# Optimization experiments

Measured on AMD Instinct MI355X. Metric: run time of the kernel, lower is better.

## Reference

```python
import jax, jax.numpy as jnp
import numpy as np

B, V, F, P = 16, 100000, 200000, 65536


def _sample_one(verts, faces, e1, e2, u):
    # verts: [V,3], faces: [F,3], e1/e2/u: [P]
    tris = verts[faces]                      # [F,3,3] irregular gather
    vec1 = tris[:, 1, :] - tris[:, 0, :]
    vec2 = tris[:, 2, :] - tris[:, 0, :]
    normals = jnp.cross(vec1, vec2)          # [F,3]
    areas = jnp.linalg.norm(normals, axis=1) / 2.0  # [F]
    # area-weighted categorical sampling via inverse CDF (deterministic given u)
    cdf = jnp.cumsum(areas)
    cdf = cdf / cdf[-1]
    idx = jnp.clip(jnp.searchsorted(jax.lax.stop_gradient(cdf), u), 0, F - 1)  # [P]
    sampled_tris = tris[idx]                 # [P,3,3]
    unit_normals = normals / (areas[:, None] * 2.0)
    sampled_normals = unit_normals[idx]      # [P,3]
    # barycentric weights (Osada et al.)
    s = jnp.sqrt(e1)
    w = jnp.stack([1.0 - s, (1.0 - e2) * s, e2 * s], axis=1)[:, :, None]  # [P,3,1]
    points = jnp.sum(sampled_tris * w, axis=1)  # [P,3]
    return points, sampled_normals


def setup_inputs() -> dict:
    key = jax.random.key(0)
    k1, k2, k3, k4, k5 = jax.random.split(key, 5)
    vertices_batch = jax.random.normal(k1, (B, V, 3), dtype=jnp.float32)
    faces_batch = jax.random.randint(k2, (B, F, 3), 0, V, dtype=jnp.int64)
    eps1 = jax.random.uniform(k3, (B, P), dtype=jnp.float32)
    eps2 = jax.random.uniform(k4, (B, P), dtype=jnp.float32)
    u = jax.random.uniform(k5, (B, P), dtype=jnp.float32)
    return {"vertices_batch": vertices_batch, "faces_batch": faces_batch,
            "eps1": eps1, "eps2": eps2, "u": u}


def reference(vertices_batch, faces_batch, eps1, eps2, u):
    points, normals = jax.vmap(_sample_one)(vertices_batch, faces_batch, eps1, eps2, u)
    return points, normals  # ([B,P,3], [B,P,3])
```

## Files before the change

kernel.cpp:

```cpp
#include <hip/hip_runtime.h>

#pragma clang fp contract(off)

#define NB 16
#define NV 100000
#define NF 200000
#define NP 65536

#define B16 16
#define NW0 12500
#define NW1 782
#define NW2 49
#define NW3 4

__device__ __forceinline__ void xcd_map(int p, int& batch, int& chunk) {
    int r = p & 15;
    batch = 2 * (r & 7) + (r >> 3);
    chunk = p >> 4;
}

__global__ void detect_kernel(const int* __restrict__ faces, int* __restrict__ flag) {
    __shared__ int any;
    if (threadIdx.x == 0) any = 0;
    __syncthreads();
    int acc = 0;
    for (int i = threadIdx.x; i < 4096; i += blockDim.x)
        acc |= faces[2 * i + 1];
    if (acc) atomicOr(&any, 1);
    __syncthreads();
    if (threadIdx.x == 0) flag[0] = (any == 0) ? 1 : 0;
}

__device__ __forceinline__ void load_face(const int* __restrict__ faces,
                                          long long fidx, int is64,
                                          int& i0, int& i1, int& i2) {
    if (is64) {
        const int* p = faces + fidx * 6;
        i0 = p[0]; i1 = p[2]; i2 = p[4];
    } else {
        const int* p = faces + fidx * 3;
        i0 = p[0]; i1 = p[1]; i2 = p[2];
    }
}

__global__ void area_kernel(const float* __restrict__ verts,
                            const int* __restrict__ faces,
                            const int* __restrict__ flag,
                            float* __restrict__ area) {
    int batch, chunk;
    xcd_map(blockIdx.x, batch, chunk);
    int i = chunk * 256 + threadIdx.x;
    if (i >= NF) return;
    int is64 = flag[0];
    size_t gid = (size_t)batch * NF + i;
    const float* vb = verts + (size_t)batch * NV * 3;
    int i0, i1, i2;
    load_face(faces, (long long)gid, is64, i0, i1, i2);
    float ax = vb[3 * i0 + 0], ay = vb[3 * i0 + 1], az = vb[3 * i0 + 2];
    float bx = vb[3 * i1 + 0], by = vb[3 * i1 + 1], bz = vb[3 * i1 + 2];
    float cx = vb[3 * i2 + 0], cy = vb[3 * i2 + 1], cz = vb[3 * i2 + 2];
    float v1x = bx - ax, v1y = by - ay, v1z = bz - az;
    float v2x = cx - ax, v2y = cy - ay, v2z = cz - az;
    float nx = fmaf(v1y, v2z, -(v1z * v2y));
    float ny = fmaf(v1z, v2x, -(v1x * v2z));
    float nz = fmaf(v1x, v2y, -(v1y * v2x));
    float ss = fmaf(nz, nz, fmaf(nx, nx, ny * ny));
    float nrm = sqrtf(ss);
    area[gid] = nrm / 2.0f;
}

__global__ void winscan_kernel(float* __restrict__ cdf, float* __restrict__ s0) {
    int batch, chunk;
    xcd_map(blockIdx.x, batch, chunk);
    int j = chunk * 256 + threadIdx.x;
    if (j >= NW0) return;
    float* base = cdf + (size_t)batch * NF + (size_t)j * B16;
    float run = 0.0f;
    #pragma unroll
    for (int p = 0; p < B16; ++p) { run = run + base[p]; base[p] = run; }
    s0[(size_t)batch * NW0 + j] = run;
}

__global__ void midscan16_kernel(const float* __restrict__ s0g, float* __restrict__ S0g) {
    __shared__ float t0[NW0];
    __shared__ float t1[NW1];
    __shared__ float t2[NW2];
    __shared__ float t3[NW3];
    int b = blockIdx.x;
    for (int i = threadIdx.x; i < NW0; i += blockDim.x)
        t0[i] = s0g[(size_t)b * NW0 + i];
    __syncthreads();
    for (int w = threadIdx.x; w < NW1; w += blockDim.x) {
        int st = w * B16, en = st + B16 < NW0 ? st + B16 : NW0;
        float run = 0.0f;
        for (int p = st; p < en; ++p) { run = run + t0[p]; t0[p] = run; }
        t1[w] = run;
    }
    __syncthreads();
    for (int w = threadIdx.x; w < NW2; w += blockDim.x) {
        int st = w * B16, en = st + B16 < NW1 ? st + B16 : NW1;
        float run = 0.0f;
        for (int p = st; p < en; ++p) { run = run + t1[p]; t1[p] = run; }
        t2[w] = run;
    }
    __syncthreads();
    for (int w = threadIdx.x; w < NW3; w += blockDim.x) {
        int st = w * B16, en = st + B16 < NW2 ? st + B16 : NW2;
        float run = 0.0f;
        for (int p = st; p < en; ++p) { run = run + t2[p]; t2[p] = run; }
        t3[w] = run;
    }
    __syncthreads();
    if (threadIdx.x == 0) {
        float run = 0.0f;
        for (int k = 0; k < NW3; ++k) { run = run + t3[k]; t3[k] = run; }
    }
    __syncthreads();
    for (int i = threadIdx.x; i < NW2; i += blockDim.x) {
        int w = i >> 4;
        float off = (w > 0) ? t3[w - 1] : 0.0f;
        t2[i] = off + t2[i];
    }
    __syncthreads();
    for (int i = threadIdx.x; i < NW1; i += blockDim.x) {
        int w = i >> 4;
        float off = (w > 0) ? t2[w - 1] : 0.0f;
        t1[i] = off + t1[i];
    }
    __syncthreads();
    for (int i = threadIdx.x; i < NW0; i += blockDim.x) {
        int w = i >> 4;
        float off = (w > 0) ? t1[w - 1] : 0.0f;
        t0[i] = off + t0[i];
    }
    __syncthreads();
    for (int i = threadIdx.x; i < NW0; i += blockDim.x)
        S0g[(size_t)b * NW0 + i] = t0[i];
}

__global__ void fused_norm_kernel(float* __restrict__ cdf,
                                  const float* __restrict__ s0,
                                  const float* __restrict__ S0) {
    int batch, chunk;
    xcd_map(blockIdx.x, batch, chunk);
    int i = chunk * 256 + threadIdx.x;
    if (i >= NF) return;
    const float* S0b = S0 + (size_t)batch * NW0;
    float total = S0b[NW0 - 2] + s0[(size_t)batch * NW0 + NW0 - 1];
    float rcp = 1.0f / total;
    int j = i >> 4;
    float off = (j > 0) ? S0b[j - 1] : 0.0f;
    float* p = cdf + (size_t)batch * NF + i;
    *p = (off + *p) * rcp;
}

__global__ void sample_kernel(const float* __restrict__ verts,
                              const int* __restrict__ faces,
                              const int* __restrict__ flag,
                              const float* __restrict__ e1,
                              const float* __restrict__ e2,
                              const float* __restrict__ u,
                              const float* __restrict__ cdf,
                              float* __restrict__ out) {
    int batch, chunk;
    xcd_map(blockIdx.x, batch, chunk);
    int li = chunk * 256 + threadIdx.x;
    int b = batch;
    int gid = (b << 16) + li;
    int is64 = flag[0];
    const float* c = cdf + (size_t)b * NF;

    float uv = u[gid];
    int low = 0, high = NF;
    #pragma unroll
    for (int it = 0; it < 18; ++it) {
        int mid = (low + high) >> 1;
        bool go_left = (uv <= c[mid]);
        low  = go_left ? low : mid;
        high = go_left ? mid : high;
    }
    int idx = high < NF - 1 ? high : NF - 1;

    const float* vb = verts + (size_t)b * NV * 3;
    int i0, i1, i2;
    load_face(faces, (long long)b * NF + idx, is64, i0, i1, i2);
    double ax = vb[3 * i0 + 0], ay = vb[3 * i0 + 1], az = vb[3 * i0 + 2];
    double bx = vb[3 * i1 + 0], by = vb[3 * i1 + 1], bz = vb[3 * i1 + 2];
    double cx = vb[3 * i2 + 0], cy = vb[3 * i2 + 1], cz = vb[3 * i2 + 2];

    double v1x = bx - ax, v1y = by - ay, v1z = bz - az;
    double v2x = cx - ax, v2y = cy - ay, v2z = cz - az;
    double nx = v1y * v2z - v1z * v2y;
    double ny = v1z * v2x - v1x * v2z;
    double nz = v1x * v2y - v1y * v2x;
    double ss = (nx * nx + ny * ny) + nz * nz;
    double nrm = sqrt(ss);
    double unx = nx / nrm, uny = ny / nrm, unz = nz / nrm;

    double s = sqrt((double)e1[gid]);
    double t = (double)e2[gid];
    double w0 = 1.0 - s;
    double w1 = (1.0 - t) * s;
    double w2 = t * s;
    double px = (ax * w0 + bx * w1) + cx * w2;
    double py = (ay * w0 + by * w1) + cy * w2;
    double pz = (az * w0 + bz * w1) + cz * w2;

    size_t po = (size_t)gid * 3;
    out[po + 0] = (float)px;
    out[po + 1] = (float)py;
    out[po + 2] = (float)pz;
    size_t no = (size_t)NB * NP * 3 + po;
    out[no + 0] = (float)unx;
    out[no + 1] = (float)uny;
    out[no + 2] = (float)unz;
}

extern "C" void kernel_launch(void* const* d_in, const int* in_sizes, int n_in,
                              void* d_out, int out_size, void* d_ws, size_t ws_size,
                              hipStream_t stream) {
    const float* verts = (const float*)d_in[0];
    const int*   faces = (const int*)d_in[1];
    const float* e1    = (const float*)d_in[2];
    const float* e2    = (const float*)d_in[3];
    const float* u     = (const float*)d_in[4];
    float* out = (float*)d_out;

    char* ws = (char*)d_ws;
    int*   flag = (int*)ws;
    float* cdf  = (float*)(ws + 512);
    float* s0   = (float*)(ws + 512 + (size_t)NB * NF * 4);
    float* S0   = (float*)(ws + 512 + (size_t)NB * NF * 4 + (size_t)NB * NW0 * 4);

    detect_kernel<<<1, 256, 0, stream>>>(faces, flag);

    area_kernel<<<16 * 782, 256, 0, stream>>>(verts, faces, flag, cdf);

    winscan_kernel<<<16 * 49, 256, 0, stream>>>(cdf, s0);

    midscan16_kernel<<<NB, 256, 0, stream>>>(s0, S0);

    fused_norm_kernel<<<16 * 782, 256, 0, stream>>>(cdf, s0, S0);

    sample_kernel<<<16 * 256, 256, 0, stream>>>(verts, faces, flag, e1, e2, u, cdf, out);
}
```

Baseline: 174.1 us.

## Fuse area and window scan; cache top binary-search levels in shared memory

Merges the area computation with the 16-element window prefix scan through shared memory, which removes one kernel launch and a read-modify-write pass over the area array. The sample kernel now builds, per block, a shared-memory table holding the first 12 levels of the implicit binary-search tree over the CDF. The first 12 search steps read that table instead of global memory, and only the last 6 steps touch global memory. The cost is that every block rebuilds the 4095-entry table with scattered global reads, and each block is only 256 threads, so this overhead is large relative to the searches it saves.

```diff
diff --git a/kernel.cpp b/kernel.cpp
--- a/kernel.cpp
+++ b/kernel.cpp
@@ -12,6 +12,9 @@
 #define NW1 782
 #define NW2 49
 #define NW3 4
+
+#define TREE_LVL 12
+#define TREE_N   (1 << TREE_LVL)
 
 __device__ __forceinline__ void xcd_map(int p, int& batch, int& chunk) {
     int r = p & 15;
@@ -43,42 +46,46 @@
     }
 }
 
-__global__ void area_kernel(const float* __restrict__ verts,
-                            const int* __restrict__ faces,
-                            const int* __restrict__ flag,
-                            float* __restrict__ area) {
+__global__ void area_prefix_kernel(const float* __restrict__ verts,
+                                   const int* __restrict__ faces,
+                                   const int* __restrict__ flag,
+                                   float* __restrict__ cdf,
+                                   float* __restrict__ s0) {
+    __shared__ float S[256];
     int batch, chunk;
     xcd_map(blockIdx.x, batch, chunk);
-    int i = chunk * 256 + threadIdx.x;
-    if (i >= NF) return;
-    int is64 = flag[0];
-    size_t gid = (size_t)batch * NF + i;
-    const float* vb = verts + (size_t)batch * NV * 3;
-    int i0, i1, i2;
-    load_face(faces, (long long)gid, is64, i0, i1, i2);
-    float ax = vb[3 * i0 + 0], ay = vb[3 * i0 + 1], az = vb[3 * i0 + 2];
-    float bx = vb[3 * i1 + 0], by = vb[3 * i1 + 1], bz = vb[3 * i1 + 2];
-    float cx = vb[3 * i2 + 0], cy = vb[3 * i2 + 1], cz = vb[3 * i2 + 2];
-    float v1x = bx - ax, v1y = by - ay, v1z = bz - az;
-    float v2x = cx - ax, v2y = cy - ay, v2z = cz - az;
-    float nx = fmaf(v1y, v2z, -(v1z * v2y));
-    float ny = fmaf(v1z, v2x, -(v1x * v2z));
-    float nz = fmaf(v1x, v2y, -(v1y * v2x));
-    float ss = fmaf(nz, nz, fmaf(nx, nx, ny * ny));
-    float nrm = sqrtf(ss);
-    area[gid] = nrm / 2.0f;
-}
-
-__global__ void winscan_kernel(float* __restrict__ cdf, float* __restrict__ s0) {
-    int batch, chunk;
-    xcd_map(blockIdx.x, batch, chunk);
-    int j = chunk * 256 + threadIdx.x;
-    if (j >= NW0) return;
-    float* base = cdf + (size_t)batch * NF + (size_t)j * B16;
-    float run = 0.0f;
-    #pragma unroll
-    for (int p = 0; p < B16; ++p) { run = run + base[p]; base[p] = run; }
-    s0[(size_t)batch * NW0 + j] = run;
+    int tid = threadIdx.x;
+    int i = chunk * 256 + tid;
+    bool valid = (i < NF);
+    float a = 0.0f;
+    if (valid) {
+        int is64 = flag[0];
+        size_t gid = (size_t)batch * NF + i;
+        const float* vb = verts + (size_t)batch * NV * 3;
+        int i0, i1, i2;
+        load_face(faces, (long long)gid, is64, i0, i1, i2);
+        float ax = vb[3 * i0 + 0], ay = vb[3 * i0 + 1], az = vb[3 * i0 + 2];
+        float bx = vb[3 * i1 + 0], by = vb[3 * i1 + 1], bz = vb[3 * i1 + 2];
+        float cx = vb[3 * i2 + 0], cy = vb[3 * i2 + 1], cz = vb[3 * i2 + 2];
+        float v1x = bx - ax, v1y = by - ay, v1z = bz - az;
+        float v2x = cx - ax, v2y = cy - ay, v2z = cz - az;
+        float nx = fmaf(v1y, v2z, -(v1z * v2y));
+        float ny = fmaf(v1z, v2x, -(v1x * v2z));
+        float nz = fmaf(v1x, v2y, -(v1y * v2x));
+        float ss = fmaf(nz, nz, fmaf(nx, nx, ny * ny));
+        float nrm = sqrtf(ss);
+        a = nrm / 2.0f;
+    }
+    S[tid] = a;
+    __syncthreads();
+    if (valid) {
+        int base = tid & ~15;
+        float run = S[base];
+        for (int p = base + 1; p <= tid; ++p) run = run + S[p];
+        cdf[(size_t)batch * NF + i] = run;
+        if ((tid & 15) == 15)
+            s0[(size_t)batch * NW0 + (i >> 4)] = run;
+    }
 }
 
 __global__ void midscan16_kernel(const float* __restrict__ s0g, float* __restrict__ S0g) {
@@ -162,22 +169,41 @@
                               const float* __restrict__ u,
                               const float* __restrict__ cdf,
                               float* __restrict__ out) {
+    __shared__ float T[TREE_N];
     int batch, chunk;
     xcd_map(blockIdx.x, batch, chunk);
+    int b = batch;
+    const float* c = cdf + (size_t)b * NF;
+
+    for (int n = 1 + threadIdx.x; n < TREE_N; n += blockDim.x) {
+        int k = 31 - __clz(n);
+        int low = 0, high = NF;
+        for (int j = k - 1; j >= 0; --j) {
+            int mid = (low + high) >> 1;
+            if ((n >> j) & 1) low = mid; else high = mid;
+        }
+        T[n] = c[(low + high) >> 1];
+    }
+    __syncthreads();
+
     int li = chunk * 256 + threadIdx.x;
-    int b = batch;
     int gid = (b << 16) + li;
     int is64 = flag[0];
-    const float* c = cdf + (size_t)b * NF;
 
     float uv = u[gid];
-    int low = 0, high = NF;
+    int low = 0, high = NF, node = 1;
     #pragma unroll
-    for (int it = 0; it < 18; ++it) {
+    for (int it = 0; it < TREE_LVL; ++it) {
         int mid = (low + high) >> 1;
-        bool go_left = (uv <= c[mid]);
-        low  = go_left ? low : mid;
-        high = go_left ? mid : high;
+        bool gl = (uv <= T[node]);
+        node = 2 * node + (gl ? 0 : 1);
+        if (gl) high = mid; else low = mid;
+    }
+    #pragma unroll
+    for (int it = TREE_LVL; it < 18; ++it) {
+        int mid = (low + high) >> 1;
+        bool gl = (uv <= c[mid]);
+        if (gl) high = mid; else low = mid;
     }
     int idx = high < NF - 1 ? high : NF - 1;
 
@@ -234,9 +260,7 @@
 
     detect_kernel<<<1, 256, 0, stream>>>(faces, flag);
 
-    area_kernel<<<16 * 782, 256, 0, stream>>>(verts, faces, flag, cdf);
-
-    winscan_kernel<<<16 * 49, 256, 0, stream>>>(cdf, s0);
+    area_prefix_kernel<<<16 * 782, 256, 0, stream>>>(verts, faces, flag, cdf, s0);
 
     midscan16_kernel<<<NB, 256, 0, stream>>>(s0, S0);
 
```

Result: slower. 200.9 us (+15.4%).
